# Optimization experiments

Measured on AMD Instinct MI355X. Metric: run time of the kernel, lower is better.

## Reference

```python
import jax, jax.numpy as jnp
import numpy as np

N, M, DIST, HEADS, D, C, DFFN = 16384, 16, 2, 8, 256, 64, 512
DH = D // HEADS
GRID = 128
BLOCK = 2048  # mirrors torch batch_size loop in find_neighboring_voxels_optimized
EPS = 1e-5


def _neighbors(coords_f, src, m, dist):
    """Blockwise Manhattan-distance topk neighbor gather.
    coords_f: (N,3) float voxel coords; src: (N,D) features.
    Returns (N, m, D) neighbor features, zero-filled where fewer than m in range."""
    n = coords_f.shape[0]
    qblocks = coords_f.reshape(-1, BLOCK, 3)

    def one_block(cb):
        # (BLOCK, N) Manhattan distances
        d = jnp.abs(cb[:, None, :] - coords_f[None, :, :]).sum(-1)
        d = jnp.where(d <= dist, d, jnp.inf)
        vals, idx = jax.lax.top_k(-d, m)          # nearest m (self first: dist 0)
        valid = (vals > -jnp.inf)[..., None]
        return jnp.where(valid, src[idx], jnp.zeros((), src.dtype))

    return jax.lax.map(one_block, qblocks).reshape(n, m, src.shape[-1])


def _layernorm(x, g, b):
    mu = x.mean(-1, keepdims=True)
    var = ((x - mu) ** 2).mean(-1, keepdims=True)
    return (x - mu) * jax.lax.rsqrt(var + EPS) * g + b


def setup_inputs() -> dict:
    key = jax.random.key(0)
    ks = jax.random.split(key, 32)
    p = lambda i, shape, s: jax.random.normal(ks[i], shape, dtype=jnp.float32) * s
    z = lambda shape: jnp.zeros(shape, dtype=jnp.float32)
    o = lambda shape: jnp.ones(shape, dtype=jnp.float32)
    return {
        "coords": jax.random.randint(ks[0], (N, 3), 0, GRID, dtype=jnp.int32),
        "features": jax.random.normal(ks[1], (N, C), dtype=jnp.float32),
        "pe_w1": p(2, (3, D // 2), 0.5), "pe_b1": z((D // 2,)),
        "pe_w2": p(3, (D // 2, D), 0.08), "pe_b2": z((D,)),
        "proj_w": p(4, (C, D), 0.12), "proj_b": z((D,)),
        "wq": p(5, (D, D), 0.06), "bq": z((D,)),
        "wk": p(6, (D, D), 0.06), "bk": z((D,)),
        "wv": p(7, (D, D), 0.06), "bv": z((D,)),
        "wo": p(8, (D, D), 0.06), "bo": z((D,)),
        "ffn_w1": p(9, (D, DFFN), 0.06), "ffn_b1": z((DFFN,)),
        "ffn_w2": p(10, (DFFN, D), 0.04), "ffn_b2": z((D,)),
        "ln_g": o((D,)), "ln_b": z((D,)),
        "fus_w1": p(11, (D, C), 0.06), "fus_b1": z((C,)),
        "fus_w2": p(12, (2 * C, C), 0.09), "fus_b2": z((C,)),
        "bn_g": o((C,)), "bn_b": z((C,)),
    }


def reference(coords, features, pe_w1, pe_b1, pe_w2, pe_b2, proj_w, proj_b,
              wq, bq, wk, bk, wv, bv, wo, bo,
              ffn_w1, ffn_b1, ffn_w2, ffn_b2, ln_g, ln_b,
              fus_w1, fus_b1, fus_w2, fus_b2, bn_g, bn_b):
    coords_f = coords.astype(jnp.float32)
    # dynamic learnable positional encoding on normalized coords
    xn = coords_f / (GRID - 1)
    pe = jax.nn.relu(xn @ pe_w1 + pe_b1) @ pe_w2 + pe_b2
    src = features @ proj_w + proj_b + pe                       # (N, D)

    nf = _neighbors(coords_f, src, M, DIST)                     # (N, M, D)
    query = nf[:, 0, :]                                         # (N, D) self-feature

    # multihead attention: query len 1, key len M, batch N
    q = (query @ wq + bq).reshape(N, HEADS, DH)
    k = (nf @ wk + bk).reshape(N, M, HEADS, DH)
    v = (nf @ wv + bv).reshape(N, M, HEADS, DH)
    scores = jnp.einsum('nhd,nmhd->nhm', q, k) / jnp.sqrt(jnp.float32(DH))
    attn = jax.nn.softmax(scores, axis=-1)
    ao = jnp.einsum('nhm,nmhd->nhd', attn, v).reshape(N, D) @ wo + bo  # (N, D)

    # FFN with residual + LayerNorm (dropout=0 / eval)
    h = jax.nn.relu(ao @ ffn_w1 + ffn_b1) @ ffn_w2 + ffn_b2
    y = _layernorm(ao + h, ln_g, ln_b)                          # (N, D)

    # EnhancedFusion: project, concat, linear, BatchNorm1d (batch stats), ReLU
    t = y @ fus_w1 + fus_b1                                     # (N, C)
    f = jnp.concatenate([features, t], axis=1) @ fus_w2 + fus_b2
    mu = f.mean(0)
    var = ((f - mu) ** 2).mean(0)
    f = (f - mu) * jax.lax.rsqrt(var + EPS) * bn_g + bn_b
    return jax.nn.relu(f)                                       # (N, C)
```

## Files before the change

### kernel.cpp

```cpp
#include <hip/hip_runtime.h>
#include <stdint.h>

typedef unsigned short u16;
typedef unsigned int   u32;
typedef __attribute__((ext_vector_type(8))) short short8;
typedef __attribute__((ext_vector_type(4))) float f32x4;

static constexpr int kN = 16384;
static constexpr float kEPS = 1e-5f;

__device__ __forceinline__ u16 f2bf(float x) {
  u32 u = __float_as_uint(x);
  u32 r = (u + 0x7fffu + ((u >> 16) & 1u)) >> 16;
  return (u16)r;
}
__device__ __forceinline__ void ldbf8(const u16* p, float* o) {
  uint4 v = *(const uint4*)p;
  o[0] = __uint_as_float(v.x << 16);  o[1] = __uint_as_float(v.x & 0xffff0000u);
  o[2] = __uint_as_float(v.y << 16);  o[3] = __uint_as_float(v.y & 0xffff0000u);
  o[4] = __uint_as_float(v.z << 16);  o[5] = __uint_as_float(v.z & 0xffff0000u);
  o[6] = __uint_as_float(v.w << 16);  o[7] = __uint_as_float(v.w & 0xffff0000u);
}


__global__ __launch_bounds__(256) void k_hist(const int* __restrict__ coords,
                                              u32* __restrict__ cnt) {
  int n = blockIdx.x * 256 + threadIdx.x;
  int c = coords[n * 3] * 128 + coords[n * 3 + 1];
  atomicAdd(&cnt[c], 1u);
}

__global__ __launch_bounds__(256) void k_scan(const u32* __restrict__ cnt,
                                              u32* __restrict__ startb) {
  __shared__ u32 tots[256];
  int t = threadIdx.x;
  int base = t * 64;
  u32 s = 0;
  for (int i = 0; i < 64; i++) s += cnt[base + i];
  tots[t] = s;
  __syncthreads();
  if (t == 0) {
    u32 run = 0;
    for (int i = 0; i < 256; i++) { u32 v = tots[i]; tots[i] = run; run += v; }
  }
  __syncthreads();
  u32 run = tots[t];
  for (int i = 0; i < 64; i++) { startb[base + i] = run; run += cnt[base + i]; }
}

__global__ __launch_bounds__(256) void k_scatter(const int* __restrict__ coords,
                                                 const u32* __restrict__ startb,
                                                 u32* __restrict__ cursor,
                                                 u32* __restrict__ pts) {
  int n = blockIdx.x * 256 + threadIdx.x;
  int x = coords[n * 3], y = coords[n * 3 + 1], z = coords[n * 3 + 2];
  int c = x * 128 + y;
  u32 slot = atomicAdd(&cursor[c], 1u);
  pts[startb[c] + slot] = ((u32)z << 14) | (u32)n;
}

__global__ __launch_bounds__(256) void k_select(const int* __restrict__ coords,
                                                const u32* __restrict__ startb,
                                                const u32* __restrict__ cnt,
                                                const u32* __restrict__ pts,
                                                int* __restrict__ idxo) {
  int n = blockIdx.x * 256 + threadIdx.x;
  int x = coords[n * 3], y = coords[n * 3 + 1], z = coords[n * 3 + 2];
  u32 best[16];
#pragma unroll
  for (int j = 0; j < 16; j++) best[j] = 0xFFFFFFFFu;
  const int dxs[13] = {0, -1, 1, 0, 0, -2, 2, 0, 0, -1, -1, 1, 1};
  const int dys[13] = {0, 0, 0, -1, 1, 0, 0, -2, 2, -1, 1, -1, 1};
  const int dbs[13] = {0, 1, 1, 1, 1, 2, 2, 2, 2, 2, 2, 2, 2};
#pragma unroll
  for (int t = 0; t < 13; t++) {
    int xx = x + dxs[t], yy = y + dys[t];
    if (xx < 0 || xx > 127 || yy < 0 || yy > 127) continue;
    int c = xx * 128 + yy;
    u32 s0 = startb[c], e0 = s0 + cnt[c];
    for (u32 i = s0; i < e0; ++i) {
      u32 p = pts[i];
      int zq = (int)(p >> 14);
      int id = (int)(p & 16383u);
      int az = z - zq; az = az < 0 ? -az : az;
      int dd = dbs[t] + az;
      u32 key = (dd <= 2) ? (((u32)dd << 14) | (u32)id) : 0xFFFFFFFFu;
#pragma unroll
      for (int j = 0; j < 16; j++) {
        u32 lo = min(best[j], key);
        u32 hi = max(best[j], key);
        best[j] = lo; key = hi;
      }
    }
  }
#pragma unroll
  for (int j = 0; j < 16; j++)
    idxo[n * 16 + j] = (best[j] == 0xFFFFFFFFu) ? -1 : (int)(best[j] & 16383u);
}

struct WSet {
  const float* s[8]; u16* d[8];
  int K[8]; int N[8]; int dstride[8]; int coff[8];
};

__global__ __launch_bounds__(256) void k_wcast(WSet ws) {
  int w = blockIdx.y;
  const float* S = ws.s[w]; u16* D = ws.d[w];
  int K = ws.K[w], N = ws.N[w], ds = ws.dstride[w], co = ws.coff[w];
  int ntx = N >> 5, tiles = ntx * (K >> 5);
  int t = blockIdx.x;
  if (t >= tiles) return;
  int n0 = (t % ntx) * 32, k0 = (t / ntx) * 32;
  __shared__ float st[32][33];
  int tr = threadIdx.x >> 3, tc4 = (threadIdx.x & 7) * 4;
  float4 v = *(const float4*)(S + (size_t)(k0 + tr) * N + n0 + tc4);
  st[tc4 + 0][tr] = v.x; st[tc4 + 1][tr] = v.y;
  st[tc4 + 2][tr] = v.z; st[tc4 + 3][tr] = v.w;
  __syncthreads();
  u16 o4[4];
  o4[0] = f2bf(st[tr][tc4 + 0]); o4[1] = f2bf(st[tr][tc4 + 1]);
  o4[2] = f2bf(st[tr][tc4 + 2]); o4[3] = f2bf(st[tr][tc4 + 3]);
  *(uint2*)(D + (size_t)(n0 + tr) * ds + co + k0 + tc4) = *(uint2*)o4;
}

__global__ __launch_bounds__(256) void k_bias2(const float* __restrict__ a,
                                               const float* __restrict__ b,
                                               float* __restrict__ o) {
  int t = threadIdx.x;
  o[t] = a[t] + b[t];
}

__global__ __launch_bounds__(320) void k_fuse2w(const float* __restrict__ uw1,
                                                const float* __restrict__ ub1,
                                                const float* __restrict__ uw2,
                                                const float* __restrict__ ub2,
                                                u16* __restrict__ W2f,
                                                float* __restrict__ bbf) {
  int n = blockIdx.x;
  int k = threadIdx.x;
  if (k < 256) {
    float s = 0.f;
    for (int j = 0; j < 64; j++) s += uw1[k * 64 + j] * uw2[(64 + j) * 64 + n];
    W2f[n * 320 + k] = f2bf(s);
  } else {
    W2f[n * 320 + k] = f2bf(uw2[(k - 256) * 64 + n]);
  }
  if (k == 0) {
    float s = ub2[n];
    for (int j = 0; j < 64; j++) s += ub1[j] * uw2[(64 + j) * 64 + n];
    bbf[n] = s;
  }
}

__global__ __launch_bounds__(256) void k_prep(const int* __restrict__ coords,
                                              const float* __restrict__ feats,
                                              const float* __restrict__ pw1,
                                              const float* __restrict__ pb1,
                                              u16* __restrict__ A1,
                                              u16* __restrict__ A2) {
  int r0 = blockIdx.x * 32;
#pragma unroll
  for (int s = 0; s < 3; s++) {
    int j = threadIdx.x + s * 256;
    int row = j / 24, seg = j % 24;
    int n = r0 + row;
    u16 o[8];
    if (seg < 8) {
      const float* fp = feats + (size_t)n * 64 + seg * 8;
      float4 a = *(const float4*)fp;
      float4 b = *(const float4*)(fp + 4);
      o[0] = f2bf(a.x); o[1] = f2bf(a.y); o[2] = f2bf(a.z); o[3] = f2bf(a.w);
      o[4] = f2bf(b.x); o[5] = f2bf(b.y); o[6] = f2bf(b.z); o[7] = f2bf(b.w);
      *(uint4*)(A2 + (size_t)n * 320 + 256 + seg * 8) = *(uint4*)o;
    } else {
      int jj0 = (seg - 8) * 8;
      float x0 = (float)coords[n * 3 + 0] * (1.f / 127.f);
      float x1 = (float)coords[n * 3 + 1] * (1.f / 127.f);
      float x2 = (float)coords[n * 3 + 2] * (1.f / 127.f);
#pragma unroll
      for (int u = 0; u < 8; u++) {
        int jj = jj0 + u;
        float hv = pb1[jj] + x0 * pw1[jj] + x1 * pw1[128 + jj] + x2 * pw1[256 + jj];
        o[u] = f2bf(fmaxf(hv, 0.f));
      }
    }
    *(uint4*)(A1 + (size_t)n * 192 + seg * 8) = *(uint4*)o;
  }
}

template <int ACT, int SF32, int SBF16, int ADD>
__global__ __launch_bounds__(256) void k_mfma_gemm(
    const u16* __restrict__ A, const u16* __restrict__ WT,
    const float* __restrict__ bias,
    float* __restrict__ Cf, u16* __restrict__ Cb,
    const float* __restrict__ Addp,
    int M, int K, int N) {
  __shared__ __align__(16) u16 As[128 * 32];
  __shared__ __align__(16) u16 Bs[128 * 32];
  const int tid = threadIdx.x;
  const int wave = tid >> 6, lane = tid & 63;
  const int bm = blockIdx.y * 128, bn = blockIdx.x * 128;
  const int wr = (wave >> 1) * 64, wc = (wave & 1) * 64;

  f32x4 acc[4][4];
#pragma unroll
  for (int i = 0; i < 4; i++)
#pragma unroll
    for (int j = 0; j < 4; j++)
#pragma unroll
      for (int r = 0; r < 4; r++) acc[i][j][r] = 0.f;

  for (int k0 = 0; k0 < K; k0 += 32) {
#pragma unroll
    for (int i = 0; i < 2; i++) {
      int cb = i * 256 + wave * 64;
      int c = cb + lane;
      int row = c >> 2, ko = (c & 3) * 8;
      int rowb = min(row, N - 1 - bn);
      __builtin_amdgcn_global_load_lds(
          (const __attribute__((address_space(1))) void*)(A + (size_t)(bm + row) * K + k0 + ko),
          (__attribute__((address_space(3))) void*)(As + (size_t)cb * 8), 16, 0, 0);
      __builtin_amdgcn_global_load_lds(
          (const __attribute__((address_space(1))) void*)(WT + (size_t)(bn + rowb) * K + k0 + ko),
          (__attribute__((address_space(3))) void*)(Bs + (size_t)cb * 8), 16, 0, 0);
    }
    __syncthreads();
    short8 af[4], bg[4];
#pragma unroll
    for (int i = 0; i < 4; i++)
      af[i] = *(const short8*)&As[(wr + i * 16 + (lane & 15)) * 32 + (lane >> 4) * 8];
#pragma unroll
    for (int j = 0; j < 4; j++)
      bg[j] = *(const short8*)&Bs[(wc + j * 16 + (lane & 15)) * 32 + (lane >> 4) * 8];
#pragma unroll
    for (int i = 0; i < 4; i++)
#pragma unroll
      for (int j = 0; j < 4; j++)
        acc[i][j] = __builtin_amdgcn_mfma_f32_16x16x32_bf16(af[i], bg[j], acc[i][j], 0, 0, 0);
    __syncthreads();
  }

#pragma unroll
  for (int j = 0; j < 4; j++) {
    int cc = bn + wc + j * 16 + (lane & 15);
    if (cc >= N) continue;
    float bval = bias ? bias[cc] : 0.f;
#pragma unroll
    for (int i = 0; i < 4; i++) {
      int rbase = bm + wr + i * 16 + (lane >> 4) * 4;
#pragma unroll
      for (int r = 0; r < 4; r++) {
        float v = acc[i][j][r] + bval;
        size_t o = (size_t)(rbase + r) * N + cc;
        if (ADD) v += Addp[o];
        if (ACT) v = fmaxf(v, 0.f);
        if (SF32) Cf[o] = v;
        if (SBF16) Cb[o] = f2bf(v);
      }
    }
  }
}

__global__ __launch_bounds__(256) void k_attn(const u16* __restrict__ QKV,
                                              const u32* __restrict__ pts,
                                              const int* __restrict__ idx,
                                              const float* __restrict__ bq,
                                              const float* __restrict__ bk,
                                              const float* __restrict__ bv,
                                              u16* __restrict__ outp) {
  int gid = blockIdx.x * 256 + threadIdx.x;
  int n = (int)(pts[gid >> 3] & 16383u), h = gid & 7;
  const int* ip = idx + n * 16;
  const int hb = h * 32;
  float q[32];
  {
    int i0 = ip[0];
    const u16* qp = QKV + (size_t)i0 * 768 + hb;
#pragma unroll
    for (int j = 0; j < 32; j += 8) ldbf8(qp + j, &q[j]);
#pragma unroll
    for (int j = 0; j < 32; j++) q[j] += bq[hb + j];
  }
  float qbk = 0.f;
#pragma unroll
  for (int j = 0; j < 32; j++) qbk += q[j] * bk[hb + j];
  float s[16]; int ii[16];
#pragma unroll
  for (int m = 0; m < 16; m++) {
    int i = ip[m]; ii[m] = i;
    float d = qbk;
    if (i >= 0) {
      const u16* kp = QKV + (size_t)i * 768 + 256 + hb;
      float kv[32];
#pragma unroll
      for (int j = 0; j < 32; j += 8) ldbf8(kp + j, &kv[j]);
#pragma unroll
      for (int j = 0; j < 32; j++) d += q[j] * kv[j];
    }
    s[m] = d * 0.17677669529663689f;
  }
  float mx = s[0];
#pragma unroll
  for (int m = 1; m < 16; m++) mx = fmaxf(mx, s[m]);
  float sum = 0.f;
#pragma unroll
  for (int m = 0; m < 16; m++) { s[m] = __expf(s[m] - mx); sum += s[m]; }
  float inv = 1.f / sum;
  float o[32];
#pragma unroll
  for (int j = 0; j < 32; j++) o[j] = 0.f;
#pragma unroll
  for (int m = 0; m < 16; m++) {
    if (ii[m] >= 0) {
      const u16* vp = QKV + (size_t)ii[m] * 768 + 512 + hb;
      float vv[32];
#pragma unroll
      for (int j = 0; j < 32; j += 8) ldbf8(vp + j, &vv[j]);
#pragma unroll
      for (int j = 0; j < 32; j++) o[j] += s[m] * vv[j];
    }
  }
  u16* op = outp + (size_t)n * 256 + hb;
#pragma unroll
  for (int j = 0; j < 32; j += 8) {
    u16 tmp[8];
#pragma unroll
    for (int jj = 0; jj < 8; jj++) tmp[jj] = f2bf(o[j + jj] * inv + bv[hb + j + jj]);
    *(uint4*)(op + j) = *(uint4*)tmp;
  }
}

__global__ __launch_bounds__(256) void k_ln(const float* __restrict__ xx,
                                            const float* __restrict__ g,
                                            const float* __restrict__ b,
                                            u16* __restrict__ A2) {
  int row = blockIdx.x * 4 + (threadIdx.x >> 6);
  int lane = threadIdx.x & 63;
  float4 a = *(const float4*)(xx + (size_t)row * 256 + lane * 4);
  float x0 = a.x, x1 = a.y, x2 = a.z, x3 = a.w;
  float sm = x0 + x1 + x2 + x3;
#pragma unroll
  for (int off = 1; off < 64; off <<= 1) sm += __shfl_xor(sm, off);
  float mu = sm * (1.f / 256.f);
  float d0 = x0 - mu, d1 = x1 - mu, d2 = x2 - mu, d3 = x3 - mu;
  float sq = d0 * d0 + d1 * d1 + d2 * d2 + d3 * d3;
#pragma unroll
  for (int off = 1; off < 64; off <<= 1) sq += __shfl_xor(sq, off);
  float rstd = rsqrtf(sq * (1.f / 256.f) + kEPS);
  float4 gv = *(const float4*)(g + lane * 4);
  float4 bv4 = *(const float4*)(b + lane * 4);
  u16 o[4];
  o[0] = f2bf(d0 * rstd * gv.x + bv4.x); o[1] = f2bf(d1 * rstd * gv.y + bv4.y);
  o[2] = f2bf(d2 * rstd * gv.z + bv4.z); o[3] = f2bf(d3 * rstd * gv.w + bv4.w);
  *(uint2*)(A2 + (size_t)row * 320 + lane * 4) = *(uint2*)o;
}

__global__ __launch_bounds__(256) void k_stats(const float* __restrict__ f,
                                               float* __restrict__ pS, float* __restrict__ pQ) {
  int col = threadIdx.x & 63, rc = threadIdx.x >> 6;
  int r0 = blockIdx.x * 128 + rc * 32;
  float s = 0.f, q = 0.f;
  for (int r = 0; r < 32; r++) {
    float v = f[(size_t)(r0 + r) * 64 + col];
    s += v; q += v * v;
  }
  __shared__ float ls[4][64], lq[4][64];
  ls[rc][col] = s; lq[rc][col] = q;
  __syncthreads();
  if (rc == 0) {
    s = ls[0][col] + ls[1][col] + ls[2][col] + ls[3][col];
    q = lq[0][col] + lq[1][col] + lq[2][col] + lq[3][col];
    pS[blockIdx.x * 64 + col] = s;
    pQ[blockIdx.x * 64 + col] = q;
  }
}

__global__ __launch_bounds__(64) void k_bnfin(const float* __restrict__ pS,
                                              const float* __restrict__ pQ,
                                              const float* __restrict__ g,
                                              const float* __restrict__ b,
                                              float* __restrict__ coef,
                                              float* __restrict__ shift) {
  int c = threadIdx.x;
  float s = 0.f, q = 0.f;
  for (int i = 0; i < 128; i++) { s += pS[i * 64 + c]; q += pQ[i * 64 + c]; }
  float mu = s * (1.f / 16384.f);
  float var = q * (1.f / 16384.f) - mu * mu;
  float cf = rsqrtf(var + kEPS) * g[c];
  coef[c] = cf;
  shift[c] = b[c] - mu * cf;
}

__global__ __launch_bounds__(256) void k_bnapply(const float* __restrict__ f,
                                                 const float* __restrict__ coef,
                                                 const float* __restrict__ shift,
                                                 float* __restrict__ out) {
  int gid = blockIdx.x * 256 + threadIdx.x;
  int e = gid * 4, col = e & 63;
  float4 v = *(const float4*)(f + e);
  float4 cf = *(const float4*)(coef + col);
  float4 sh = *(const float4*)(shift + col);
  float4 o;
  o.x = fmaxf(v.x * cf.x + sh.x, 0.f);
  o.y = fmaxf(v.y * cf.y + sh.y, 0.f);
  o.z = fmaxf(v.z * cf.z + sh.z, 0.f);
  o.w = fmaxf(v.w * cf.w + sh.w, 0.f);
  *(float4*)(out + e) = o;
}

extern "C" void kernel_launch(void* const* d_in, const int* in_sizes, int n_in,
                              void* d_out, int out_size, void* d_ws, size_t ws_size,
                              hipStream_t stream) {
  (void)in_sizes; (void)n_in; (void)out_size; (void)ws_size;
  const int*   coords = (const int*)d_in[0];
  const float* feats  = (const float*)d_in[1];
  const float* pe_w1  = (const float*)d_in[2];
  const float* pe_b1  = (const float*)d_in[3];
  const float* pe_w2  = (const float*)d_in[4];
  const float* pe_b2  = (const float*)d_in[5];
  const float* proj_w = (const float*)d_in[6];
  const float* proj_b = (const float*)d_in[7];
  const float* wq  = (const float*)d_in[8];
  const float* bq  = (const float*)d_in[9];
  const float* wk  = (const float*)d_in[10];
  const float* bk  = (const float*)d_in[11];
  const float* wv  = (const float*)d_in[12];
  const float* bv  = (const float*)d_in[13];
  const float* wo  = (const float*)d_in[14];
  const float* bo  = (const float*)d_in[15];
  const float* fw1 = (const float*)d_in[16];
  const float* fb1 = (const float*)d_in[17];
  const float* fw2 = (const float*)d_in[18];
  const float* fb2 = (const float*)d_in[19];
  const float* lng = (const float*)d_in[20];
  const float* lnb = (const float*)d_in[21];
  const float* uw1 = (const float*)d_in[22];
  const float* ub1 = (const float*)d_in[23];
  const float* uw2 = (const float*)d_in[24];
  const float* ub2 = (const float*)d_in[25];
  const float* bng = (const float*)d_in[26];
  const float* bnb = (const float*)d_in[27];
  float* out = (float*)d_out;

  char* Wc = (char*)d_ws;
  const size_t MB = 1u << 20;
  u16*   A1    = (u16*)(Wc + 0 * MB);
  u16*   srcb  = (u16*)(Wc + 6 * MB);
  u16*   QKVb  = (u16*)(Wc + 14 * MB);
  u16*   aoInB = (u16*)(Wc + 38 * MB);
  float* aoF   = (float*)(Wc + 46 * MB);
  u16*   aoB   = (u16*)(Wc + 62 * MB);
  u16*   h1B   = (u16*)(Wc + 70 * MB);
  u16*   A2    = (u16*)(Wc + 86 * MB);
  float* xB    = (float*)(Wc + 14 * MB);
  float* fB    = (float*)(Wc + 0 * MB);

  u16* qkvT  = (u16*)(Wc + 96 * MB);
  u16* woT   = qkvT + 196608;
  u16* fw1T  = woT + 65536;
  u16* fw2T  = fw1T + 131072;
  u16* W1T   = fw2T + 131072;
  u16* W2f   = W1T + 49152;
  float* pbc = (float*)(W2f + 20480);
  float* bbf = pbc + 256;

  u32* cnt    = (u32*)(Wc + 98 * MB);
  u32* cursor = cnt + 16384;
  u32* startb = cnt + 32768;
  u32* pts    = cnt + 49152;
  int* idxb   = (int*)(cnt + 65536);
  float* pS    = (float*)(cnt + 65536 + 262144);
  float* pQ    = pS + 8192;
  float* coefb = pQ + 8192;
  float* shb   = coefb + 64;

  hipMemsetAsync(cnt, 0, 32768 * sizeof(u32), stream);

  k_hist<<<64, 256, 0, stream>>>(coords, cnt);
  k_scan<<<1, 256, 0, stream>>>(cnt, startb);
  k_scatter<<<64, 256, 0, stream>>>(coords, startb, cursor, pts);
  k_select<<<64, 256, 0, stream>>>(coords, startb, cnt, pts, idxb);

  WSet ws;
  ws.s[0] = wq;     ws.d[0] = qkvT;          ws.K[0] = 256; ws.N[0] = 256; ws.dstride[0] = 256; ws.coff[0] = 0;
  ws.s[1] = wk;     ws.d[1] = qkvT + 65536;  ws.K[1] = 256; ws.N[1] = 256; ws.dstride[1] = 256; ws.coff[1] = 0;
  ws.s[2] = wv;     ws.d[2] = qkvT + 131072; ws.K[2] = 256; ws.N[2] = 256; ws.dstride[2] = 256; ws.coff[2] = 0;
  ws.s[3] = wo;     ws.d[3] = woT;           ws.K[3] = 256; ws.N[3] = 256; ws.dstride[3] = 256; ws.coff[3] = 0;
  ws.s[4] = fw1;    ws.d[4] = fw1T;          ws.K[4] = 256; ws.N[4] = 512; ws.dstride[4] = 256; ws.coff[4] = 0;
  ws.s[5] = fw2;    ws.d[5] = fw2T;          ws.K[5] = 512; ws.N[5] = 256; ws.dstride[5] = 512; ws.coff[5] = 0;
  ws.s[6] = proj_w; ws.d[6] = W1T;           ws.K[6] = 64;  ws.N[6] = 256; ws.dstride[6] = 192; ws.coff[6] = 0;
  ws.s[7] = pe_w2;  ws.d[7] = W1T;           ws.K[7] = 128; ws.N[7] = 256; ws.dstride[7] = 192; ws.coff[7] = 64;
  k_wcast<<<dim3(128, 8), 256, 0, stream>>>(ws);
  k_bias2<<<1, 256, 0, stream>>>(proj_b, pe_b2, pbc);
  k_fuse2w<<<64, 320, 0, stream>>>(uw1, ub1, uw2, ub2, W2f, bbf);

  k_prep<<<512, 256, 0, stream>>>(coords, feats, pe_w1, pe_b1, A1, A2);

  k_mfma_gemm<0, 0, 1, 0><<<dim3(2, 128), 256, 0, stream>>>(A1, W1T, pbc, nullptr, srcb, nullptr, kN, 192, 256);
  k_mfma_gemm<0, 0, 1, 0><<<dim3(6, 128), 256, 0, stream>>>(srcb, qkvT, nullptr, nullptr, QKVb, nullptr, kN, 256, 768);

  k_attn<<<512, 256, 0, stream>>>(QKVb, pts, idxb, bq, bk, bv, aoInB);

  k_mfma_gemm<0, 1, 1, 0><<<dim3(2, 128), 256, 0, stream>>>(aoInB, woT, bo, aoF, aoB, nullptr, kN, 256, 256);
  k_mfma_gemm<1, 0, 1, 0><<<dim3(4, 128), 256, 0, stream>>>(aoB, fw1T, fb1, nullptr, h1B, nullptr, kN, 256, 512);
  k_mfma_gemm<0, 1, 0, 1><<<dim3(2, 128), 256, 0, stream>>>(h1B, fw2T, fb2, xB, nullptr, aoF, kN, 512, 256);

  k_ln<<<4096, 256, 0, stream>>>(xB, lng, lnb, A2);

  k_mfma_gemm<0, 1, 0, 0><<<dim3(1, 128), 256, 0, stream>>>(A2, W2f, bbf, fB, nullptr, nullptr, kN, 320, 64);

  k_stats<<<128, 256, 0, stream>>>(fB, pS, pQ);
  k_bnfin<<<1, 64, 0, stream>>>(pS, pQ, bng, bnb, coefb, shb);
  k_bnapply<<<1024, 256, 0, stream>>>(fB, coefb, shb, out);
}
```

Baseline: 268.0 us.

## Shrink GEMM tiles to 64x64, merge setup kernels, keep intermediates in bf16

The GEMM template now takes its tile size as a parameter, and every GEMM launches with 64x64 tiles, which gives more blocks across the CUs. The weight cast, bias sum, fused fusion weights and the memset of the histogram counters are merged into one k_setup launch, removing several small launches. The attention output residual and the FFN output now stay in bf16 rather than fp32, which halves their traffic but adds rounding error before the layernorm. The column bounds check in the GEMM is dropped, and smaller tiles mean less data reuse per block.

Result: faster. 257.6 us (-3.9%).

```diff
diff --git a/kernel.cpp b/kernel.cpp
--- a/kernel.cpp
+++ b/kernel.cpp
@@ -13,6 +13,9 @@
   u32 u = __float_as_uint(x);
   u32 r = (u + 0x7fffu + ((u >> 16) & 1u)) >> 16;
   return (u16)r;
+}
+__device__ __forceinline__ float bf2f(u16 x) {
+  return __uint_as_float(((u32)x) << 16);
 }
 __device__ __forceinline__ void ldbf8(const u16* p, float* o) {
   uint4 v = *(const uint4*)p;
@@ -103,8 +106,41 @@
   int K[8]; int N[8]; int dstride[8]; int coff[8];
 };
 
-__global__ __launch_bounds__(256) void k_wcast(WSet ws) {
+__global__ __launch_bounds__(256) void k_setup(WSet ws,
+                                               u32* __restrict__ zero_area,
+                                               const float* __restrict__ proj_b,
+                                               const float* __restrict__ pe_b2,
+                                               float* __restrict__ pbc,
+                                               const float* __restrict__ uw1,
+                                               const float* __restrict__ ub1,
+                                               const float* __restrict__ uw2,
+                                               const float* __restrict__ ub2,
+                                               u16* __restrict__ W2f,
+                                               float* __restrict__ bbf) {
   int w = blockIdx.y;
+  if (w == 8) {
+    zero_area[blockIdx.x * 256 + threadIdx.x] = 0u;
+    return;
+  }
+  if (w == 9) {
+    int bx = blockIdx.x;
+    if (bx == 0) {
+      pbc[threadIdx.x] = proj_b[threadIdx.x] + pe_b2[threadIdx.x];
+    } else if (bx < 65) {
+      int n = bx - 1;
+      int k = threadIdx.x;
+      float s = 0.f;
+      for (int j = 0; j < 64; j++) s += uw1[k * 64 + j] * uw2[(64 + j) * 64 + n];
+      W2f[n * 320 + k] = f2bf(s);
+      if (k < 64) W2f[n * 320 + 256 + k] = f2bf(uw2[k * 64 + n]);
+      if (k == 0) {
+        float b = ub2[n];
+        for (int j = 0; j < 64; j++) b += ub1[j] * uw2[(64 + j) * 64 + n];
+        bbf[n] = b;
+      }
+    }
+    return;
+  }
   const float* S = ws.s[w]; u16* D = ws.d[w];
   int K = ws.K[w], N = ws.N[w], ds = ws.dstride[w], co = ws.coff[w];
   int ntx = N >> 5, tiles = ntx * (K >> 5);
@@ -121,35 +157,6 @@
   o4[0] = f2bf(st[tr][tc4 + 0]); o4[1] = f2bf(st[tr][tc4 + 1]);
   o4[2] = f2bf(st[tr][tc4 + 2]); o4[3] = f2bf(st[tr][tc4 + 3]);
   *(uint2*)(D + (size_t)(n0 + tr) * ds + co + k0 + tc4) = *(uint2*)o4;
-}
-
-__global__ __launch_bounds__(256) void k_bias2(const float* __restrict__ a,
-                                               const float* __restrict__ b,
-                                               float* __restrict__ o) {
-  int t = threadIdx.x;
-  o[t] = a[t] + b[t];
-}
-
-__global__ __launch_bounds__(320) void k_fuse2w(const float* __restrict__ uw1,
-                                                const float* __restrict__ ub1,
-                                                const float* __restrict__ uw2,
-                                                const float* __restrict__ ub2,
-                                                u16* __restrict__ W2f,
-                                                float* __restrict__ bbf) {
-  int n = blockIdx.x;
-  int k = threadIdx.x;
-  if (k < 256) {
-    float s = 0.f;
-    for (int j = 0; j < 64; j++) s += uw1[k * 64 + j] * uw2[(64 + j) * 64 + n];
-    W2f[n * 320 + k] = f2bf(s);
-  } else {
-    W2f[n * 320 + k] = f2bf(uw2[(k - 256) * 64 + n]);
-  }
-  if (k == 0) {
-    float s = ub2[n];
-    for (int j = 0; j < 64; j++) s += ub1[j] * uw2[(64 + j) * 64 + n];
-    bbf[n] = s;
-  }
 }
 
 __global__ __launch_bounds__(256) void k_prep(const int* __restrict__ coords,
@@ -188,74 +195,80 @@
   }
 }
 
-template <int ACT, int SF32, int SBF16, int ADD>
+template <int BM, int BN, int ACT, int OUTBF, int ADD>
 __global__ __launch_bounds__(256) void k_mfma_gemm(
     const u16* __restrict__ A, const u16* __restrict__ WT,
     const float* __restrict__ bias,
-    float* __restrict__ Cf, u16* __restrict__ Cb,
-    const float* __restrict__ Addp,
+    void* __restrict__ Cout,
+    const u16* __restrict__ Addp,
     int M, int K, int N) {
-  __shared__ __align__(16) u16 As[128 * 32];
-  __shared__ __align__(16) u16 Bs[128 * 32];
+  constexpr int GA = BM / 64;
+  constexpr int GT = (BM + BN) / 64;
+  constexpr int AI = BM / 32;
+  constexpr int BI = BN / 32;
+  __shared__ __align__(16) u16 As[BM * 32];
+  __shared__ __align__(16) u16 Bs[BN * 32];
   const int tid = threadIdx.x;
   const int wave = tid >> 6, lane = tid & 63;
-  const int bm = blockIdx.y * 128, bn = blockIdx.x * 128;
-  const int wr = (wave >> 1) * 64, wc = (wave & 1) * 64;
-
-  f32x4 acc[4][4];
-#pragma unroll
-  for (int i = 0; i < 4; i++)
-#pragma unroll
-    for (int j = 0; j < 4; j++)
+  const int bm = blockIdx.y * BM, bn = blockIdx.x * BN;
+  const int wr = (wave >> 1) * (BM / 2), wc = (wave & 1) * (BN / 2);
+
+  f32x4 acc[AI][BI];
+#pragma unroll
+  for (int i = 0; i < AI; i++)
+#pragma unroll
+    for (int j = 0; j < BI; j++)
 #pragma unroll
       for (int r = 0; r < 4; r++) acc[i][j][r] = 0.f;
 
   for (int k0 = 0; k0 < K; k0 += 32) {
 #pragma unroll
-    for (int i = 0; i < 2; i++) {
-      int cb = i * 256 + wave * 64;
-      int c = cb + lane;
-      int row = c >> 2, ko = (c & 3) * 8;
-      int rowb = min(row, N - 1 - bn);
-      __builtin_amdgcn_global_load_lds(
-          (const __attribute__((address_space(1))) void*)(A + (size_t)(bm + row) * K + k0 + ko),
-          (__attribute__((address_space(3))) void*)(As + (size_t)cb * 8), 16, 0, 0);
-      __builtin_amdgcn_global_load_lds(
-          (const __attribute__((address_space(1))) void*)(WT + (size_t)(bn + rowb) * K + k0 + ko),
-          (__attribute__((address_space(3))) void*)(Bs + (size_t)cb * 8), 16, 0, 0);
+    for (int i = 0; i < GT; i++) {
+      int g = i * 256 + wave * 64 + lane;
+      if (i < GA) {
+        int row = g >> 2, ko = (g & 3) * 8;
+        __builtin_amdgcn_global_load_lds(
+            (const __attribute__((address_space(1))) void*)(A + (size_t)(bm + row) * K + k0 + ko),
+            (__attribute__((address_space(3))) void*)(As + (size_t)g * 8), 16, 0, 0);
+      } else {
+        int g2 = g - GA * 256;
+        int row = g2 >> 2, ko = (g2 & 3) * 8;
+        __builtin_amdgcn_global_load_lds(
+            (const __attribute__((address_space(1))) void*)(WT + (size_t)(bn + row) * K + k0 + ko),
+            (__attribute__((address_space(3))) void*)(Bs + (size_t)g2 * 8), 16, 0, 0);
+      }
     }
     __syncthreads();
-    short8 af[4], bg[4];
-#pragma unroll
-    for (int i = 0; i < 4; i++)
+    short8 af[AI], bg[BI];
+#pragma unroll
+    for (int i = 0; i < AI; i++)
       af[i] = *(const short8*)&As[(wr + i * 16 + (lane & 15)) * 32 + (lane >> 4) * 8];
 #pragma unroll
-    for (int j = 0; j < 4; j++)
+    for (int j = 0; j < BI; j++)
       bg[j] = *(const short8*)&Bs[(wc + j * 16 + (lane & 15)) * 32 + (lane >> 4) * 8];
 #pragma unroll
-    for (int i = 0; i < 4; i++)
-#pragma unroll
-      for (int j = 0; j < 4; j++)
+    for (int i = 0; i < AI; i++)
+#pragma unroll
+      for (int j = 0; j < BI; j++)
         acc[i][j] = __builtin_amdgcn_mfma_f32_16x16x32_bf16(af[i], bg[j], acc[i][j], 0, 0, 0);
     __syncthreads();
   }
 
 #pragma unroll
-  for (int j = 0; j < 4; j++) {
+  for (int j = 0; j < BI; j++) {
     int cc = bn + wc + j * 16 + (lane & 15);
-    if (cc >= N) continue;
     float bval = bias ? bias[cc] : 0.f;
 #pragma unroll
-    for (int i = 0; i < 4; i++) {
+    for (int i = 0; i < AI; i++) {
       int rbase = bm + wr + i * 16 + (lane >> 4) * 4;
 #pragma unroll
       for (int r = 0; r < 4; r++) {
         float v = acc[i][j][r] + bval;
         size_t o = (size_t)(rbase + r) * N + cc;
-        if (ADD) v += Addp[o];
+        if (ADD) v += bf2f(Addp[o]);
         if (ACT) v = fmaxf(v, 0.f);
-        if (SF32) Cf[o] = v;
-        if (SBF16) Cb[o] = f2bf(v);
+        if (OUTBF) ((u16*)Cout)[o] = f2bf(v);
+        else       ((float*)Cout)[o] = v;
       }
     }
   }
@@ -330,14 +343,15 @@
   }
 }
 
-__global__ __launch_bounds__(256) void k_ln(const float* __restrict__ xx,
+__global__ __launch_bounds__(256) void k_ln(const u16* __restrict__ xx,
                                             const float* __restrict__ g,
                                             const float* __restrict__ b,
                                             u16* __restrict__ A2) {
   int row = blockIdx.x * 4 + (threadIdx.x >> 6);
   int lane = threadIdx.x & 63;
-  float4 a = *(const float4*)(xx + (size_t)row * 256 + lane * 4);
-  float x0 = a.x, x1 = a.y, x2 = a.z, x3 = a.w;
+  uint2 raw = *(const uint2*)(xx + (size_t)row * 256 + lane * 4);
+  float x0 = __uint_as_float(raw.x << 16), x1 = __uint_as_float(raw.x & 0xffff0000u);
+  float x2 = __uint_as_float(raw.y << 16), x3 = __uint_as_float(raw.y & 0xffff0000u);
   float sm = x0 + x1 + x2 + x3;
 #pragma unroll
   for (int off = 1; off < 64; off <<= 1) sm += __shfl_xor(sm, off);
@@ -448,11 +462,10 @@
   u16*   srcb  = (u16*)(Wc + 6 * MB);
   u16*   QKVb  = (u16*)(Wc + 14 * MB);
   u16*   aoInB = (u16*)(Wc + 38 * MB);
-  float* aoF   = (float*)(Wc + 46 * MB);
-  u16*   aoB   = (u16*)(Wc + 62 * MB);
-  u16*   h1B   = (u16*)(Wc + 70 * MB);
-  u16*   A2    = (u16*)(Wc + 86 * MB);
-  float* xB    = (float*)(Wc + 14 * MB);
+  u16*   aoB   = (u16*)(Wc + 46 * MB);
+  u16*   h1B   = (u16*)(Wc + 54 * MB);
+  u16*   xBb   = (u16*)(Wc + 70 * MB);
+  u16*   A2    = (u16*)(Wc + 78 * MB);
   float* fB    = (float*)(Wc + 0 * MB);
 
   u16* qkvT  = (u16*)(Wc + 96 * MB);
@@ -474,13 +487,6 @@
   float* coefb = pQ + 8192;
   float* shb   = coefb + 64;
 
-  hipMemsetAsync(cnt, 0, 32768 * sizeof(u32), stream);
-
-  k_hist<<<64, 256, 0, stream>>>(coords, cnt);
-  k_scan<<<1, 256, 0, stream>>>(cnt, startb);
-  k_scatter<<<64, 256, 0, stream>>>(coords, startb, cursor, pts);
-  k_select<<<64, 256, 0, stream>>>(coords, startb, cnt, pts, idxb);
-
   WSet ws;
   ws.s[0] = wq;     ws.d[0] = qkvT;          ws.K[0] = 256; ws.N[0] = 256; ws.dstride[0] = 256; ws.coff[0] = 0;
   ws.s[1] = wk;     ws.d[1] = qkvT + 65536;  ws.K[1] = 256; ws.N[1] = 256; ws.dstride[1] = 256; ws.coff[1] = 0;
@@ -490,24 +496,28 @@
   ws.s[5] = fw2;    ws.d[5] = fw2T;          ws.K[5] = 512; ws.N[5] = 256; ws.dstride[5] = 512; ws.coff[5] = 0;
   ws.s[6] = proj_w; ws.d[6] = W1T;           ws.K[6] = 64;  ws.N[6] = 256; ws.dstride[6] = 192; ws.coff[6] = 0;
   ws.s[7] = pe_w2;  ws.d[7] = W1T;           ws.K[7] = 128; ws.N[7] = 256; ws.dstride[7] = 192; ws.coff[7] = 64;
-  k_wcast<<<dim3(128, 8), 256, 0, stream>>>(ws);
-  k_bias2<<<1, 256, 0, stream>>>(proj_b, pe_b2, pbc);
-  k_fuse2w<<<64, 320, 0, stream>>>(uw1, ub1, uw2, ub2, W2f, bbf);
+  k_setup<<<dim3(128, 10), 256, 0, stream>>>(ws, cnt, proj_b, pe_b2, pbc,
+                                             uw1, ub1, uw2, ub2, W2f, bbf);
+
+  k_hist<<<64, 256, 0, stream>>>(coords, cnt);
+  k_scan<<<1, 256, 0, stream>>>(cnt, startb);
+  k_scatter<<<64, 256, 0, stream>>>(coords, startb, cursor, pts);
+  k_select<<<64, 256, 0, stream>>>(coords, startb, cnt, pts, idxb);
 
   k_prep<<<512, 256, 0, stream>>>(coords, feats, pe_w1, pe_b1, A1, A2);
 
-  k_mfma_gemm<0, 0, 1, 0><<<dim3(2, 128), 256, 0, stream>>>(A1, W1T, pbc, nullptr, srcb, nullptr, kN, 192, 256);
-  k_mfma_gemm<0, 0, 1, 0><<<dim3(6, 128), 256, 0, stream>>>(srcb, qkvT, nullptr, nullptr, QKVb, nullptr, kN, 256, 768);
+  k_mfma_gemm<64, 64, 0, 1, 0><<<dim3(4, 256), 256, 0, stream>>>(A1, W1T, pbc, srcb, nullptr, kN, 192, 256);
+  k_mfma_gemm<64, 64, 0, 1, 0><<<dim3(12, 256), 256, 0, stream>>>(srcb, qkvT, nullptr, QKVb, nullptr, kN, 256, 768);
 
   k_attn<<<512, 256, 0, stream>>>(QKVb, pts, idxb, bq, bk, bv, aoInB);
 
-  k_mfma_gemm<0, 1, 1, 0><<<dim3(2, 128), 256, 0, stream>>>(aoInB, woT, bo, aoF, aoB, nullptr, kN, 256, 256);
-  k_mfma_gemm<1, 0, 1, 0><<<dim3(4, 128), 256, 0, stream>>>(aoB, fw1T, fb1, nullptr, h1B, nullptr, kN, 256, 512);
-  k_mfma_gemm<0, 1, 0, 1><<<dim3(2, 128), 256, 0, stream>>>(h1B, fw2T, fb2, xB, nullptr, aoF, kN, 512, 256);
-
-  k_ln<<<4096, 256, 0, stream>>>(xB, lng, lnb, A2);
-
-  k_mfma_gemm<0, 1, 0, 0><<<dim3(1, 128), 256, 0, stream>>>(A2, W2f, bbf, fB, nullptr, nullptr, kN, 320, 64);
+  k_mfma_gemm<64, 64, 0, 1, 0><<<dim3(4, 256), 256, 0, stream>>>(aoInB, woT, bo, aoB, nullptr, kN, 256, 256);
+  k_mfma_gemm<64, 64, 1, 1, 0><<<dim3(8, 256), 256, 0, stream>>>(aoB, fw1T, fb1, h1B, nullptr, kN, 256, 512);
+  k_mfma_gemm<64, 64, 0, 1, 1><<<dim3(4, 256), 256, 0, stream>>>(h1B, fw2T, fb2, xBb, aoB, kN, 512, 256);
+
+  k_ln<<<4096, 256, 0, stream>>>(xBb, lng, lnb, A2);
+
+  k_mfma_gemm<64, 64, 0, 0, 0><<<dim3(1, 256), 256, 0, stream>>>(A2, W2f, bbf, fB, nullptr, kN, 320, 64);
 
   k_stats<<<128, 256, 0, stream>>>(fB, pS, pQ);
   k_bnfin<<<1, 64, 0, stream>>>(pS, pQ, bng, bnb, coefb, shb);
```
